# Kernel optimization log

Hardware: AMD Instinct MI355X
Metric: run time of the kernel (lower is better)

## Reference

```python
import jax, jax.numpy as jnp
import numpy as np

SEQ, BATCH, EMBED, HIDDEN = 2048, 64, 256, 256


def setup_inputs() -> dict:
    key = jax.random.key(0)
    ks = jax.random.split(key, 13)
    bound = 1.0 / np.sqrt(HIDDEN)
    u = lambda k, shape: jax.random.uniform(k, shape, jnp.float32, -bound, bound)
    inp = {
        "embeds": jax.random.normal(ks[0], (SEQ, BATCH, EMBED), jnp.float32),
        "W_ix": u(ks[1], (EMBED, HIDDEN)), "W_ih": u(ks[2], (HIDDEN, HIDDEN)), "b_i": u(ks[3], (HIDDEN,)),
        "W_fx": u(ks[4], (EMBED, HIDDEN)), "W_fh": u(ks[5], (HIDDEN, HIDDEN)), "b_f": u(ks[6], (HIDDEN,)) + 1.0,
        "W_gx": u(ks[7], (EMBED, HIDDEN)), "W_gh": u(ks[8], (HIDDEN, HIDDEN)), "b_g": u(ks[9], (HIDDEN,)),
        "W_ox": u(ks[10], (EMBED, HIDDEN)), "W_oh": u(ks[11], (HIDDEN, HIDDEN)), "b_o": u(ks[12], (HIDDEN,)),
    }
    return inp


def reference(embeds, W_ix, W_ih, b_i, W_fx, W_fh, b_f, W_gx, W_gh, b_g, W_ox, W_oh, b_o):
    # Precompute input projections for all timesteps (one big GEMM each),
    # matching x_t @ W_*x + b_* inside the loop.
    xi = embeds @ W_ix + b_i  # [S, B, H]
    xf = embeds @ W_fx + b_f
    xg = embeds @ W_gx + b_g
    xo = embeds @ W_ox + b_o

    def step(carry, x):
        h, c = carry
        xi_t, xf_t, xg_t, xo_t = x
        i_t = jax.nn.sigmoid(xi_t + h @ W_ih)
        f_t = jax.nn.sigmoid(xf_t + h @ W_fh)
        g_t = jnp.tanh(xg_t + h @ W_gh)
        o_t = jax.nn.sigmoid(xo_t + h @ W_oh)
        c = f_t * c + i_t * g_t
        h = o_t * jnp.tanh(c)
        return (h, c), h

    B = embeds.shape[1]
    h0 = jnp.zeros((B, W_ih.shape[0]), embeds.dtype)
    c0 = jnp.zeros_like(h0)
    _, out = jax.lax.scan(step, (h0, c0), (xi, xf, xg, xo))
    return out  # [S, B, H]
```

## Files before the change

kernel.cpp:

```cpp
#include <hip/hip_runtime.h>

typedef _Float16 f16;
typedef _Float16 f16x8 __attribute__((ext_vector_type(8)));
typedef float    f32x4 __attribute__((ext_vector_type(4)));

#define SEQ   2048
#define BATCH 64
#define EMBED 256
#define HID   256
#define NC    1024

__device__ __forceinline__ float fexp2(float x){ float r; asm("v_exp_f32 %0, %1" : "=v"(r) : "v"(x)); return r; }
__device__ __forceinline__ float frcp (float x){ float r; asm("v_rcp_f32 %0, %1" : "=v"(r) : "v"(x)); return r; }
__device__ __forceinline__ float sigm_f(float y){ return frcp(1.f + fexp2(y * -1.44269504f)); }
__device__ __forceinline__ float tanh_f(float y){ return 2.f*frcp(1.f + fexp2(y * -2.88539009f)) - 1.f; }

__device__ __forceinline__ void gload_lds4(const void* g, void* s) {
  __builtin_amdgcn_global_load_lds((const __attribute__((address_space(1))) void*)g,
                                   (__attribute__((address_space(3))) void*)s, 4, 0, 0);
}

__global__ __launch_bounds__(256) void prep_w(
    const float* __restrict__ Wix, const float* __restrict__ Wih,
    const float* __restrict__ Wfx, const float* __restrict__ Wfh,
    const float* __restrict__ Wgx, const float* __restrict__ Wgh,
    const float* __restrict__ Wox, const float* __restrict__ Woh,
    f16* __restrict__ Wx_t, f16* __restrict__ Wh_t, f16* __restrict__ Wfrag)
{
  int tid = blockIdx.x*256 + threadIdx.x;
  const float* WX[4] = {Wix, Wfx, Wgx, Wox};
  const float* WH[4] = {Wih, Wfh, Wgh, Woh};
  if (tid < 65536) {
    int which = tid >> 15;
    int j  = (tid >> 5) & 1023;
    int ko = tid & 31;
    const float* src = (which ? WH : WX)[j >> 8];
    int u = j & 255;
    f16x8 v;
    #pragma unroll
    for (int q = 0; q < 8; ++q) v[q] = (f16)src[(ko*8+q)*HID + u];
    *(f16x8*)((which ? Wh_t : Wx_t) + (size_t)j*256 + ko*8) = v;
  } else if (tid < 65536 + 8192) {
    int r   = tid - 65536;
    int l   = r & 63, gt = (r >> 6) & 63, kfi = r >> 12;
    int col = gt*16 + (l & 15);
    int kbase = 192 + kfi*32 + (l >> 4)*8;
    const float* src = WH[col >> 8];
    int u = col & 255;
    f16x8 v;
    #pragma unroll
    for (int q = 0; q < 8; ++q) v[q] = (f16)src[(kbase+q)*HID + u];
    *(f16x8*)(Wfrag + (size_t)r*8) = v;
  }
}

__global__ __launch_bounds__(256) void gemm_x(
    const float* __restrict__ emb, const f16* __restrict__ Bt,
    const float* __restrict__ b0, const float* __restrict__ b1,
    const float* __restrict__ b2, const float* __restrict__ b3,
    f16* __restrict__ Xo)
{
  __shared__ f16 Al[64*256];
  __shared__ f16 Bl[64*256];
  int wg = blockIdx.x;
  int R0 = (wg >> 4) * 64;
  int C0 = (wg & 15) * 64;
  int tid = threadIdx.x;

  #pragma unroll
  for (int j = 0; j < 8; ++j) {
    int c = tid + j*256; int row = c >> 5, ci = c & 31;
    const float* ap = emb + (size_t)(R0+row)*EMBED + ci*8;
    f32x4 a0 = *(const f32x4*)ap;
    f32x4 a1 = *(const f32x4*)(ap + 4);
    f16x8 v;
    #pragma unroll
    for (int q = 0; q < 4; ++q) { v[q] = (f16)a0[q]; v[q+4] = (f16)a1[q]; }
    *(f16x8*)((char*)Al + row*512 + ((ci*16) ^ ((row&7)<<4))) = v;
    f16x8 vb = *(const f16x8*)(Bt + (size_t)(C0+row)*256 + ci*8);
    *(f16x8*)((char*)Bl + row*512 + ((ci*16) ^ ((row&7)<<4))) = vb;
  }
  __syncthreads();

  int w = tid >> 6, l = tid & 63, lr = l & 15, lg = l >> 4;
  const float* bp = (C0 < 256) ? b0 : (C0 < 512) ? b1 : (C0 < 768) ? b2 : b3;
  int ub = (C0 & 255) + lr;
  f32x4 cf[4];
  #pragma unroll
  for (int nt = 0; nt < 4; ++nt) { float bv = bp[ub + nt*16]; cf[nt] = (f32x4){bv,bv,bv,bv}; }

  #pragma unroll
  for (int kf = 0; kf < 8; ++kf) {
    int arow = w*16 + lr;
    f16x8 af = *(const f16x8*)((char*)Al + arow*512 + ((kf*64 + lg*16) ^ ((arow&7)<<4)));
    #pragma unroll
    for (int nt = 0; nt < 4; ++nt) {
      int brow = nt*16 + lr;
      f16x8 bf = *(const f16x8*)((char*)Bl + brow*512 + ((kf*64 + lg*16) ^ ((brow&7)<<4)));
      cf[nt] = __builtin_amdgcn_mfma_f32_16x16x32_f16(af, bf, cf[nt], 0, 0, 0);
    }
  }
  #pragma unroll
  for (int nt = 0; nt < 4; ++nt)
    #pragma unroll
    for (int r = 0; r < 4; ++r) {
      int row = R0 + w*16 + lg*4 + r;
      int col = C0 + nt*16 + lr;
      Xo[(size_t)row*NC + col] = (f16)cf[nt][r];
    }
}

__global__ __attribute__((amdgpu_flat_work_group_size(512,512), amdgpu_waves_per_eu(2,2)))
void lstm_rec(
    const f16* __restrict__ Wh_t, const f16* __restrict__ Wfrag,
    const f16* __restrict__ X, float* __restrict__ out)
{
  __shared__ f16 Wl[65536];
  __shared__ f16 hbuf[2][256];
  __shared__ f16 xl[3][1024];

  int b   = blockIdx.x;
  int tid = threadIdx.x;
  int w = tid >> 6, l = tid & 63, lr = l & 15, lg = l >> 4;

  gload_lds4(X + (size_t)b*NC + tid*2,           &xl[0][w*128]);
  gload_lds4(X + (size_t)(BATCH + b)*NC + tid*2, &xl[1][w*128]);

  {
    const f16x8* srcp = (const f16x8*)Wfrag;
    f16x8* dstp = (f16x8*)Wl;
    #pragma unroll
    for (int i = 0; i < 16; ++i) dstp[tid + i*512] = srcp[tid + i*512];
  }
  f16x8 WB[8][6];
  #pragma unroll
  for (int nt = 0; nt < 8; ++nt) {
    int col = (nt>>1)*256 + w*32 + (nt&1)*16 + lr;
    const f16* basep = Wh_t + (size_t)col*256 + lg*8;
    #pragma unroll
    for (int kf = 0; kf < 6; ++kf) WB[nt][kf] = *(const f16x8*)(basep + kf*32);
  }
  #pragma unroll
  for (int nt = 0; nt < 8; ++nt)
    #pragma unroll
    for (int kf = 0; kf < 6; ++kf)
      asm volatile("" : "+v"(WB[nt][kf]));

  ((f16*)hbuf)[tid] = (f16)0.f;
  float cA = 0.f, cB = 0.f;

  asm volatile("s_waitcnt vmcnt(0) lgkmcnt(0)" ::: "memory");
  __builtin_amdgcn_s_barrier();

  int xc = 0;
  for (int t = 0; t < SEQ; ++t) {
    int cur = t & 1;
    if (t + 2 < SEQ) {
      int xn2 = (xc == 0) ? 2 : xc - 1;
      gload_lds4(X + ((size_t)(t+2)*BATCH + b)*NC + tid*2, &xl[xn2][w*128]);
    }
    const f16* xp = xl[xc];
    f32x4 cf[8];
    #pragma unroll
    for (int nt = 0; nt < 8; ++nt) {
      float xv = (float)xp[(nt>>1)*256 + w*32 + (nt&1)*16 + lr];
      cf[nt] = (f32x4){xv, xv, xv, xv};
    }
    #pragma unroll
    for (int kf = 0; kf < 6; ++kf) {
      f16x8 ha = *(const f16x8*)(&hbuf[cur][kf*32 + lg*8]);
      #pragma unroll
      for (int nt = 0; nt < 8; ++nt)
        cf[nt] = __builtin_amdgcn_mfma_f32_16x16x32_f16(ha, WB[nt][kf], cf[nt], 0, 0, 0);
    }
    #pragma unroll
    for (int kfi = 0; kfi < 2; ++kfi) {
      f16x8 ha = *(const f16x8*)(&hbuf[cur][(6+kfi)*32 + lg*8]);
      #pragma unroll
      for (int nt = 0; nt < 8; ++nt) {
        int tau = (nt>>1)*16 + w*2 + (nt&1);
        f16x8 wb = *(const f16x8*)(&Wl[(size_t)((kfi*64 + tau)*64 + l)*8]);
        cf[nt] = __builtin_amdgcn_mfma_f32_16x16x32_f16(ha, wb, cf[nt], 0, 0, 0);
      }
    }
    if (l < 16) {
      float iA = sigm_f(cf[0][0]), iB = sigm_f(cf[1][0]);
      float fA = sigm_f(cf[2][0]), fB = sigm_f(cf[3][0]);
      float gA = tanh_f(cf[4][0]), gB = tanh_f(cf[5][0]);
      float oA = sigm_f(cf[6][0]), oB = sigm_f(cf[7][0]);
      cA = fA*cA + iA*gA;
      cB = fB*cB + iB*gB;
      float hA = oA*tanh_f(cA);
      float hB = oB*tanh_f(cB);
      int uA = w*32 + lr, uB = uA + 16;
      hbuf[cur^1][uA] = (f16)hA;
      hbuf[cur^1][uB] = (f16)hB;
      float* op = out + ((size_t)t*BATCH + b)*HID;
      op[uA] = hA;
      op[uB] = hB;
    }
    asm volatile("s_waitcnt vmcnt(3) lgkmcnt(0)" ::: "memory");
    __builtin_amdgcn_s_barrier();

    xc = (xc == 2) ? 0 : xc + 1;
  }
}

extern "C" void kernel_launch(void* const* d_in, const int* in_sizes, int n_in,
                              void* d_out, int out_size, void* d_ws, size_t ws_size,
                              hipStream_t stream) {
  const float* emb = (const float*)d_in[0];
  const float* Wix = (const float*)d_in[1];
  const float* Wih = (const float*)d_in[2];
  const float* bi  = (const float*)d_in[3];
  const float* Wfx = (const float*)d_in[4];
  const float* Wfh = (const float*)d_in[5];
  const float* bf  = (const float*)d_in[6];
  const float* Wgx = (const float*)d_in[7];
  const float* Wgh = (const float*)d_in[8];
  const float* bg  = (const float*)d_in[9];
  const float* Wox = (const float*)d_in[10];
  const float* Woh = (const float*)d_in[11];
  const float* bo  = (const float*)d_in[12];

  char* ws = (char*)d_ws;
  f16* Wx_t  = (f16*)(ws);
  f16* Wh_t  = (f16*)(ws + 524288);
  f16* Wfrag = (f16*)(ws + 1048576);
  f16* Xp    = (f16*)(ws + 1179648);

  prep_w  <<<288,   256, 0, stream>>>(Wix, Wih, Wfx, Wfh, Wgx, Wgh, Wox, Woh,
                                      Wx_t, Wh_t, Wfrag);
  gemm_x  <<<32768, 256, 0, stream>>>(emb, Wx_t, bi, bf, bg, bo, Xp);
  lstm_rec<<<64,    512, 0, stream>>>(Wh_t, Wfrag, Xp, (float*)d_out);
}
```

Baseline: 4.655 ms.

## Rebalance recurrent weight fragments across registers, LDS and global, deepen x prefetch

The recurrent weight tiles are split three ways per wave: 38 MFMA fragments stay in registers, 12 are staged in a smaller LDS region, and the remaining fragments are re-read from global memory (L2) every timestep. The per-timestep input projections are now prefetched four steps ahead into a five-slot LDS ring instead of two ahead into three slots. The explicit vmcnt wait before the barrier is dropped. The aim is to cut register pressure and LDS footprint, at the cost of extra global-load latency on the serial critical path of each step. It also relies on the waits the compiler inserts for the later weight loads to make sure the prefetched x data has landed.

Result: slower. 7.609 ms (+63.5%).

```diff
diff --git a/kernel.cpp b/kernel.cpp
--- a/kernel.cpp
+++ b/kernel.cpp
@@ -40,16 +40,20 @@
     #pragma unroll
     for (int q = 0; q < 8; ++q) v[q] = (f16)src[(ko*8+q)*HID + u];
     *(f16x8*)((which ? Wh_t : Wx_t) + (size_t)j*256 + ko*8) = v;
-  } else if (tid < 65536 + 8192) {
-    int r   = tid - 65536;
-    int l   = r & 63, gt = (r >> 6) & 63, kfi = r >> 12;
-    int col = gt*16 + (l & 15);
-    int kbase = 192 + kfi*32 + (l >> 4)*8;
+  } else if (tid < 65536 + 6144) {
+    int r  = tid - 65536;
+    int l  = r & 63;
+    int fi = (r >> 6) % 12;
+    int w  = r / 768;
+    int nt = (fi < 8) ? 5 : 6;
+    int kf = (fi < 8) ? fi : fi - 8;
+    int col = (nt>>1)*256 + w*32 + (nt&1)*16 + (l & 15);
+    int k0  = kf*32 + (l >> 4)*8;
     const float* src = WH[col >> 8];
     int u = col & 255;
     f16x8 v;
     #pragma unroll
-    for (int q = 0; q < 8; ++q) v[q] = (f16)src[(kbase+q)*HID + u];
+    for (int q = 0; q < 8; ++q) v[q] = (f16)src[(k0+q)*HID + u];
     *(f16x8*)(Wfrag + (size_t)r*8) = v;
   }
 }
@@ -111,42 +115,43 @@
 }
 
 __global__ __attribute__((amdgpu_flat_work_group_size(512,512), amdgpu_waves_per_eu(2,2)))
-void lstm_rec(
-    const f16* __restrict__ Wh_t, const f16* __restrict__ Wfrag,
-    const f16* __restrict__ X, float* __restrict__ out)
+void lstm_rec(f16* Wh_t, const f16* __restrict__ Wfrag,
+              const f16* __restrict__ X, float* out)
 {
-  __shared__ f16 Wl[65536];
+  __shared__ f16 Wl[8*12*64*8];
   __shared__ f16 hbuf[2][256];
-  __shared__ f16 xl[3][1024];
-
-  int b   = blockIdx.x;
-  int tid = threadIdx.x;
+  __shared__ f16 xl[5][1024];
+
+  int b = blockIdx.x, tid = threadIdx.x;
   int w = tid >> 6, l = tid & 63, lr = l & 15, lg = l >> 4;
 
-  gload_lds4(X + (size_t)b*NC + tid*2,           &xl[0][w*128]);
-  gload_lds4(X + (size_t)(BATCH + b)*NC + tid*2, &xl[1][w*128]);
+  #pragma unroll
+  for (int q = 0; q < 4; ++q)
+    gload_lds4(X + (size_t)(q*BATCH + b)*NC + w*128 + l*2, &xl[q][w*128]);
 
   {
     const f16x8* srcp = (const f16x8*)Wfrag;
     f16x8* dstp = (f16x8*)Wl;
     #pragma unroll
-    for (int i = 0; i < 16; ++i) dstp[tid + i*512] = srcp[tid + i*512];
-  }
-  f16x8 WB[8][6];
-  #pragma unroll
-  for (int nt = 0; nt < 8; ++nt) {
+    for (int i = 0; i < 12; ++i) dstp[tid + i*512] = srcp[tid + i*512];
+  }
+  f16x8 WB[38];
+  #pragma unroll
+  for (int nt = 0; nt < 5; ++nt) {
     int col = (nt>>1)*256 + w*32 + (nt&1)*16 + lr;
-    const f16* basep = Wh_t + (size_t)col*256 + lg*8;
-    #pragma unroll
-    for (int kf = 0; kf < 6; ++kf) WB[nt][kf] = *(const f16x8*)(basep + kf*32);
-  }
-  #pragma unroll
-  for (int nt = 0; nt < 8; ++nt)
-    #pragma unroll
-    for (int kf = 0; kf < 6; ++kf)
-      asm volatile("" : "+v"(WB[nt][kf]));
-
-  ((f16*)hbuf)[tid] = (f16)0.f;
+    f16* basep = Wh_t + (size_t)col*256 + lg*8;
+    #pragma unroll
+    for (int kf = 0; kf < 8; ++kf)
+      if (nt < 4 || kf < 6) WB[nt*8+kf] = *(f16x8*)(basep + kf*32);
+  }
+  #pragma unroll
+  for (int i = 0; i < 38; ++i) asm volatile("" : "+v"(WB[i]));
+
+  f16* whb4 = Wh_t + (size_t)(2*256 + w*32 + 0*16 + lr)*256 + lg*8;
+  f16* whb6 = Wh_t + (size_t)(3*256 + w*32 + 0*16 + lr)*256 + lg*8;
+  f16* whb7 = Wh_t + (size_t)(3*256 + w*32 + 1*16 + lr)*256 + lg*8;
+
+  if (tid < 256) ((unsigned*)hbuf)[tid] = 0;
   float cA = 0.f, cB = 0.f;
 
   asm volatile("s_waitcnt vmcnt(0) lgkmcnt(0)" ::: "memory");
@@ -155,10 +160,6 @@
   int xc = 0;
   for (int t = 0; t < SEQ; ++t) {
     int cur = t & 1;
-    if (t + 2 < SEQ) {
-      int xn2 = (xc == 0) ? 2 : xc - 1;
-      gload_lds4(X + ((size_t)(t+2)*BATCH + b)*NC + tid*2, &xl[xn2][w*128]);
-    }
     const f16* xp = xl[xc];
     f32x4 cf[8];
     #pragma unroll
@@ -167,21 +168,26 @@
       cf[nt] = (f32x4){xv, xv, xv, xv};
     }
     #pragma unroll
-    for (int kf = 0; kf < 6; ++kf) {
+    for (int kf = 0; kf < 8; ++kf) {
       f16x8 ha = *(const f16x8*)(&hbuf[cur][kf*32 + lg*8]);
       #pragma unroll
-      for (int nt = 0; nt < 8; ++nt)
-        cf[nt] = __builtin_amdgcn_mfma_f32_16x16x32_f16(ha, WB[nt][kf], cf[nt], 0, 0, 0);
-    }
-    #pragma unroll
-    for (int kfi = 0; kfi < 2; ++kfi) {
-      f16x8 ha = *(const f16x8*)(&hbuf[cur][(6+kfi)*32 + lg*8]);
-      #pragma unroll
       for (int nt = 0; nt < 8; ++nt) {
-        int tau = (nt>>1)*16 + w*2 + (nt&1);
-        f16x8 wb = *(const f16x8*)(&Wl[(size_t)((kfi*64 + tau)*64 + l)*8]);
+        f16x8 wb;
+        if (nt < 4 || (nt == 4 && kf < 6)) {
+          wb = WB[nt*8+kf];
+        } else if (nt == 5 || (nt == 6 && kf < 4)) {
+          int fi = (nt == 5) ? kf : 8 + kf;
+          wb = *(const f16x8*)(&Wl[(size_t)((w*12 + fi)*64 + l)*8]);
+        } else {
+          f16* bp = (nt == 4) ? whb4 : (nt == 6) ? whb6 : whb7;
+          wb = *(f16x8*)(bp + kf*32);
+        }
         cf[nt] = __builtin_amdgcn_mfma_f32_16x16x32_f16(ha, wb, cf[nt], 0, 0, 0);
       }
+    }
+    if (t + 4 < SEQ) {
+      int xn = xc + 4; if (xn >= 5) xn -= 5;
+      gload_lds4(X + ((size_t)(t+4)*BATCH + b)*NC + w*128 + l*2, &xl[xn][w*128]);
     }
     if (l < 16) {
       float iA = sigm_f(cf[0][0]), iB = sigm_f(cf[1][0]);
@@ -199,10 +205,10 @@
       op[uA] = hA;
       op[uB] = hB;
     }
-    asm volatile("s_waitcnt vmcnt(3) lgkmcnt(0)" ::: "memory");
+    asm volatile("s_waitcnt lgkmcnt(0)" ::: "memory");
     __builtin_amdgcn_s_barrier();
 
-    xc = (xc == 2) ? 0 : xc + 1;
+    xc = (xc == 4) ? 0 : xc + 1;
   }
 }
 
@@ -229,7 +235,7 @@
   f16* Wfrag = (f16*)(ws + 1048576);
   f16* Xp    = (f16*)(ws + 1179648);
 
-  prep_w  <<<288,   256, 0, stream>>>(Wix, Wih, Wfx, Wfh, Wgx, Wgh, Wox, Woh,
+  prep_w  <<<280,   256, 0, stream>>>(Wix, Wih, Wfx, Wfh, Wgx, Wgh, Wox, Woh,
                                       Wx_t, Wh_t, Wfrag);
   gemm_x  <<<32768, 256, 0, stream>>>(emb, Wx_t, bi, bf, bg, bo, Xp);
   lstm_rec<<<64,    512, 0, stream>>>(Wh_t, Wfrag, Xp, (float*)d_out);
```
